# Optimization experiments

Measured on AMD Instinct MI355X. Metric: run time of the kernel, lower is better.

## Reference

```python
import jax, jax.numpy as jnp
import numpy as np

IN_F, OUT_F = 128, 128
R, LEV, N = 2, 2, 8192
JD = (R - 1) * LEV + 1  # 3 filter levels


def setup_inputs() -> dict:
    key = jax.random.key(0)
    ks = jax.random.split(key, 7)
    x = jax.random.normal(ks[0], (N, IN_F), dtype=jnp.float32)
    d_list = jax.random.uniform(ks[1], (JD, N), dtype=jnp.float32)
    U = jax.random.normal(ks[2], (N, N), dtype=jnp.float32)
    Vt = jax.random.normal(ks[3], (N, N), dtype=jnp.float32)
    # learned params
    bound = float(np.sqrt(6.0 / (IN_F + OUT_F)))  # xavier_uniform
    weight = jax.random.uniform(ks[4], (IN_F, OUT_F), dtype=jnp.float32, minval=-bound, maxval=bound)
    filt = jax.random.uniform(ks[5], (JD, N), dtype=jnp.float32, minval=0.9, maxval=1.1)
    bias = jnp.zeros((OUT_F,), dtype=jnp.float32)
    return {"x": x, "d_list": d_list, "U": U, "Vt": Vt, "weight": weight, "filt": filt, "bias": bias}


def reference(x, d_list, U, Vt, weight, filt, bias):
    # Original loop: sum_j U @ ((d_j * f_j * d_j)[:, None] * (Vt @ (x @ W)))
    # By linearity this equals U @ ((sum_j d_j^2 * f_j)[:, None] * (Vt @ (x @ W)))
    # -- same math, with Vt@xw computed once and U applied once.
    xw = x @ weight                                  # [N, out]
    Vxw = Vt @ xw                                    # [N, out]
    scale = jnp.sum(d_list * filt * d_list, axis=0)  # [N]
    out = U @ (scale[:, None] * Vxw)                 # [N, out]
    return out + bias
```

## Files before the change

### kernel.cpp

```cpp
#include <hip/hip_runtime.h>

typedef short s8v __attribute__((ext_vector_type(8)));
typedef float f32x4 __attribute__((ext_vector_type(4)));

#define BM 64
#define KC 64
#define PAD 72

#define LDS_BARRIER() asm volatile("s_waitcnt lgkmcnt(0)\n\ts_barrier" ::: "memory")

__device__ __forceinline__ unsigned short f2bf(float x) {
    unsigned int u = __float_as_uint(x);
    u += 0x7fffu + ((u >> 16) & 1u);
    return (unsigned short)(u >> 16);
}

__global__ __launch_bounds__(256, 2) void gemm_kernel(
    const float* __restrict__ A, int lda,
    const unsigned short* __restrict__ Bt, int ldb,
    float* __restrict__ C, int klen)
{
    __shared__ __align__(16) unsigned short As[2][BM * PAD];
    __shared__ __align__(16) unsigned short Bs[2][128 * PAD];

    const int t    = threadIdx.x;
    const int w    = t >> 6;
    const int lane = t & 63;
    const int quad = lane >> 4;
    const int l16  = lane & 15;
    const int w32  = w * 32;
    const int kq   = quad * 8;

    const int mbase = blockIdx.x * BM;
    const int k0    = blockIdx.y * klen;
    C += (size_t)blockIdx.y * gridDim.x * BM * 128;

    const int ar = t >> 2;
    const int ak = (t & 3) * 16;
    const int br = t >> 1;
    const int bk = (t & 1) * 32;
    const float*          Ap = A  + (size_t)(mbase + ar) * lda + k0 + ak;
    const unsigned short* Bp = Bt + (size_t)br * ldb + k0 + bk;

    const int nchunks = klen / KC;

    float4 a_r[2][4];
    s8v    b_r[2][4];

    {
        #pragma unroll
        for (int i = 0; i < 4; ++i) a_r[0][i] = *(const float4*)(Ap + i * 4);
        #pragma unroll
        for (int i = 0; i < 4; ++i) b_r[0][i] = *(const s8v*)(Bp + i * 8);
        s8v v0, v1;
        v0[0] = (short)f2bf(a_r[0][0].x); v0[1] = (short)f2bf(a_r[0][0].y);
        v0[2] = (short)f2bf(a_r[0][0].z); v0[3] = (short)f2bf(a_r[0][0].w);
        v0[4] = (short)f2bf(a_r[0][1].x); v0[5] = (short)f2bf(a_r[0][1].y);
        v0[6] = (short)f2bf(a_r[0][1].z); v0[7] = (short)f2bf(a_r[0][1].w);
        v1[0] = (short)f2bf(a_r[0][2].x); v1[1] = (short)f2bf(a_r[0][2].y);
        v1[2] = (short)f2bf(a_r[0][2].z); v1[3] = (short)f2bf(a_r[0][2].w);
        v1[4] = (short)f2bf(a_r[0][3].x); v1[5] = (short)f2bf(a_r[0][3].y);
        v1[6] = (short)f2bf(a_r[0][3].z); v1[7] = (short)f2bf(a_r[0][3].w);
        *(s8v*)&As[0][ar * PAD + ak]     = v0;
        *(s8v*)&As[0][ar * PAD + ak + 8] = v1;
        #pragma unroll
        for (int i = 0; i < 4; ++i) *(s8v*)&Bs[0][br * PAD + bk + 8 * i] = b_r[0][i];
        if (nchunks > 1) {
            #pragma unroll
            for (int i = 0; i < 4; ++i) a_r[1][i] = *(const float4*)(Ap + KC + i * 4);
            #pragma unroll
            for (int i = 0; i < 4; ++i) b_r[1][i] = *(const s8v*)(Bp + KC + i * 8);
        }
    }
    LDS_BARRIER();

    f32x4 acc[4][2];
    #pragma unroll
    for (int rt = 0; rt < 4; ++rt)
        #pragma unroll
        for (int ct = 0; ct < 2; ++ct)
            acc[rt][ct] = (f32x4){0.f, 0.f, 0.f, 0.f};

#define GITER(p)                                                               \
    {                                                                          \
        if (c + 2 < nchunks) {                     \
            const size_t o = (size_t)(c + 2) * KC;                             \
            _Pragma("unroll")                                                  \
            for (int i = 0; i < 4; ++i) a_r[p][i] = *(const float4*)(Ap + o + i * 4); \
            _Pragma("unroll")                                                  \
            for (int i = 0; i < 4; ++i) b_r[p][i] = *(const s8v*)(Bp + o + i * 8);    \
        }                                                                      \
        {                                                \
            const unsigned short* as = As[p];                                  \
            const unsigned short* bs = Bs[p];                                  \
            _Pragma("unroll")                                                  \
            for (int kk = 0; kk < 2; ++kk) {                                   \
                const int ko = kk * 32 + kq;                                   \
                s8v af[4], bf[2];                                              \
                _Pragma("unroll")                                              \
                for (int rt = 0; rt < 4; ++rt)                                 \
                    af[rt] = *(const s8v*)&as[(rt * 16 + l16) * PAD + ko];     \
                _Pragma("unroll")                                              \
                for (int ct = 0; ct < 2; ++ct)                                 \
                    bf[ct] = *(const s8v*)&bs[(w32 + ct * 16 + l16) * PAD + ko]; \
                _Pragma("unroll")                                              \
                for (int rt = 0; rt < 4; ++rt)                                 \
                    _Pragma("unroll")                                          \
                    for (int ct = 0; ct < 2; ++ct)                             \
                        acc[rt][ct] = __builtin_amdgcn_mfma_f32_16x16x32_bf16( \
                            af[rt], bf[ct], acc[rt][ct], 0, 0, 0);             \
            }                                                                  \
        }                                                                      \
        if (c + 1 < nchunks) {   \
            const int q = (p) ^ 1;                                             \
            s8v v0, v1;                                                        \
            v0[0] = (short)f2bf(a_r[q][0].x); v0[1] = (short)f2bf(a_r[q][0].y);\
            v0[2] = (short)f2bf(a_r[q][0].z); v0[3] = (short)f2bf(a_r[q][0].w);\
            v0[4] = (short)f2bf(a_r[q][1].x); v0[5] = (short)f2bf(a_r[q][1].y);\
            v0[6] = (short)f2bf(a_r[q][1].z); v0[7] = (short)f2bf(a_r[q][1].w);\
            v1[0] = (short)f2bf(a_r[q][2].x); v1[1] = (short)f2bf(a_r[q][2].y);\
            v1[2] = (short)f2bf(a_r[q][2].z); v1[3] = (short)f2bf(a_r[q][2].w);\
            v1[4] = (short)f2bf(a_r[q][3].x); v1[5] = (short)f2bf(a_r[q][3].y);\
            v1[6] = (short)f2bf(a_r[q][3].z); v1[7] = (short)f2bf(a_r[q][3].w);\
            *(s8v*)&As[q][ar * PAD + ak]     = v0;                             \
            *(s8v*)&As[q][ar * PAD + ak + 8] = v1;                             \
            _Pragma("unroll")                                                  \
            for (int i = 0; i < 4; ++i)                                        \
                *(s8v*)&Bs[q][br * PAD + bk + 8 * i] = b_r[q][i];              \
        }                                                                      \
        LDS_BARRIER();                                                         \
    }

    int c = 0;
    while (true) {
        GITER(0)
        if (++c == nchunks) break;
        GITER(1)
        if (++c == nchunks) break;
    }
#undef GITER

    #pragma unroll
    for (int rt = 0; rt < 4; ++rt) {
        const int row = mbase + rt * 16 + quad * 4;
        #pragma unroll
        for (int ct = 0; ct < 2; ++ct) {
            const int col = w32 + ct * 16 + l16;
            #pragma unroll
            for (int i = 0; i < 4; ++i)
                C[(size_t)(row + i) * 128 + col] = acc[rt][ct][i];
        }
    }
}

__global__ __launch_bounds__(256) void tkern(
    const float* __restrict__ a, int nslabs,
    const float* __restrict__ dl, const float* __restrict__ ft,
    unsigned short* __restrict__ out, int nrows, int mode)
{
    __shared__ __align__(16) unsigned short L[128 * PAD];
    const int t    = threadIdx.x;
    const int kb   = blockIdx.x * 64;
    const int kloc = t >> 2;
    const int fseg = (t & 3) * 32;
    const int k    = kb + kloc;
    const size_t slab = (size_t)nrows * 128;

    float s = 1.0f;
    if (mode) {
        float s0 = 0.f;
        #pragma unroll
        for (int j = 0; j < 3; ++j) {
            float d = dl[(size_t)j * nrows + k];
            s0 += d * d * ft[(size_t)j * nrows + k];
        }
        s = s0;
    }
    const float* ap = a + (size_t)k * 128 + fseg;
    #pragma unroll
    for (int i = 0; i < 8; ++i) {
        float4 v = *(const float4*)(ap + i * 4);
        for (int sl = 1; sl < nslabs; ++sl) {
            float4 u = *(const float4*)(ap + sl * slab + i * 4);
            v.x += u.x; v.y += u.y; v.z += u.z; v.w += u.w;
        }
        const int fb = fseg + i * 4;
        L[(fb + 0) * PAD + kloc] = f2bf(v.x * s);
        L[(fb + 1) * PAD + kloc] = f2bf(v.y * s);
        L[(fb + 2) * PAD + kloc] = f2bf(v.z * s);
        L[(fb + 3) * PAD + kloc] = f2bf(v.w * s);
    }
    __syncthreads();
    const int f    = t >> 1;
    const int half = (t & 1) * 32;
    unsigned short* op = out + (size_t)f * nrows + kb + half;
    #pragma unroll
    for (int i = 0; i < 4; ++i) {
        *(s8v*)(op + i * 8) = *(const s8v*)&L[f * PAD + half + i * 8];
    }
}

__global__ __launch_bounds__(256) void addbias_kernel(
    const float* __restrict__ p, const float* __restrict__ bias,
    float* __restrict__ out)
{
    const size_t e = ((size_t)blockIdx.x * 256 + threadIdx.x) * 4;
    const size_t slab = (size_t)8192 * 128;
    float4 r = *(const float4*)(bias + (e & 127));
    #pragma unroll
    for (int s = 0; s < 4; ++s) {
        float4 x = *(const float4*)(p + s * slab + e);
        r.x += x.x; r.y += x.y; r.z += x.z; r.w += x.w;
    }
    *(float4*)(out + e) = r;
}

extern "C" void kernel_launch(void* const* d_in, const int* in_sizes, int n_in,
                              void* d_out, int out_size, void* d_ws, size_t ws_size,
                              hipStream_t stream)
{
    const float* x  = (const float*)d_in[0];
    const float* dl = (const float*)d_in[1];
    const float* U  = (const float*)d_in[2];
    const float* Vt = (const float*)d_in[3];
    const float* W  = (const float*)d_in[4];
    const float* ft = (const float*)d_in[5];
    const float* bs = (const float*)d_in[6];
    float* out = (float*)d_out;

    const int N = 8192, F = 128;
    const int SPLITK = 4;
    char* ws = (char*)d_ws;
    unsigned short* Wt  = (unsigned short*)(ws);
    unsigned short* xwt = (unsigned short*)(ws + (64 << 10));
    unsigned short* yt  = (unsigned short*)(ws + (64 << 10) + (2 << 20));
    float* bufA = (float*)(ws + (64 << 10) + (4 << 20));
    float* bufB = (float*)(ws + (64 << 10) + (20 << 20));

    tkern<<<dim3(F / 64), 256, 0, stream>>>(W, 1, nullptr, nullptr, Wt, F, 0);
    gemm_kernel<<<dim3(N / BM, 1), 256, 0, stream>>>(x, F, Wt, F, bufA, F);
    tkern<<<dim3(N / 64), 256, 0, stream>>>(bufA, 1, nullptr, nullptr, xwt, N, 0);
    gemm_kernel<<<dim3(N / BM, SPLITK), 256, 0, stream>>>(Vt, N, xwt, N, bufB, N / SPLITK);
    tkern<<<dim3(N / 64), 256, 0, stream>>>(bufB, SPLITK, dl, ft, yt, N, 1);
    gemm_kernel<<<dim3(N / BM, SPLITK), 256, 0, stream>>>(U, N, yt, N, bufA, N / SPLITK);
    addbias_kernel<<<dim3((N * F) / (256 * 4)), 256, 0, stream>>>(bufA, bs, out);
}
```

Measured before the change: 611.9 us.

## Load GEMM fragments directly from global memory and fuse xW transpose epilogue

The GEMM kernel stops staging A and B tiles through LDS with barriers. Each wave now loads its MFMA fragments straight from global memory into registers, double-buffered, and converts A to bf16 in registers; the wave layout changes to a 2x2 split of the 64x128 tile. The x@W GEMM gets its own kernel that writes bf16 transposed output directly, which removes one transpose launch and one fp32 round trip. The trade-off is that B fragments are now read redundantly by each wave, and the global accesses are less coalesced (16 rows with 32-byte segments), all for a GEMM whose cost is dominated by streaming A at 256MB.

```diff
diff --git a/kernel.cpp b/kernel.cpp
--- a/kernel.cpp
+++ b/kernel.cpp
@@ -2,12 +2,10 @@
 
 typedef short s8v __attribute__((ext_vector_type(8)));
 typedef float f32x4 __attribute__((ext_vector_type(4)));
-
-#define BM 64
+typedef unsigned short u16x4 __attribute__((ext_vector_type(4)));
+
 #define KC 64
 #define PAD 72
-
-#define LDS_BARRIER() asm volatile("s_waitcnt lgkmcnt(0)\n\ts_barrier" ::: "memory")
 
 __device__ __forceinline__ unsigned short f2bf(float x) {
     unsigned int u = __float_as_uint(x);
@@ -15,140 +13,143 @@
     return (unsigned short)(u >> 16);
 }
 
-__global__ __launch_bounds__(256, 2) void gemm_kernel(
+__device__ __forceinline__ s8v cvt_frag(const float4 lo, const float4 hi) {
+    s8v r;
+    r[0] = (short)f2bf(lo.x); r[1] = (short)f2bf(lo.y);
+    r[2] = (short)f2bf(lo.z); r[3] = (short)f2bf(lo.w);
+    r[4] = (short)f2bf(hi.x); r[5] = (short)f2bf(hi.y);
+    r[6] = (short)f2bf(hi.z); r[7] = (short)f2bf(hi.w);
+    return r;
+}
+
+__device__ __forceinline__ void gemm_core(
     const float* __restrict__ A, int lda,
     const unsigned short* __restrict__ Bt, int ldb,
-    float* __restrict__ C, int klen)
-{
-    __shared__ __align__(16) unsigned short As[2][BM * PAD];
-    __shared__ __align__(16) unsigned short Bs[2][128 * PAD];
-
+    int mbase, int k0, int klen, f32x4 acc[2][4])
+{
     const int t    = threadIdx.x;
     const int w    = t >> 6;
     const int lane = t & 63;
     const int quad = lane >> 4;
     const int l16  = lane & 15;
-    const int w32  = w * 32;
-    const int kq   = quad * 8;
-
-    const int mbase = blockIdx.x * BM;
-    const int k0    = blockIdx.y * klen;
-    C += (size_t)blockIdx.y * gridDim.x * BM * 128;
-
-    const int ar = t >> 2;
-    const int ak = (t & 3) * 16;
-    const int br = t >> 1;
-    const int bk = (t & 1) * 32;
-    const float*          Ap = A  + (size_t)(mbase + ar) * lda + k0 + ak;
-    const unsigned short* Bp = Bt + (size_t)br * ldb + k0 + bk;
-
+    const int mh   = w >> 1;
+    const int nh   = w & 1;
+
+    const float* rA0 = A + (size_t)(mbase + mh * 32 + l16) * lda + k0 + quad * 8;
+    const float* rA1 = rA0 + (size_t)16 * lda;
+    const unsigned short* rB = Bt + (size_t)(nh * 64 + l16) * ldb + k0 + quad * 8;
+    const size_t bstep = (size_t)16 * ldb;
+
+    float4 a[2][2][2][2];
+    s8v    b[2][2][4];
     const int nchunks = klen / KC;
 
-    float4 a_r[2][4];
-    s8v    b_r[2][4];
-
-    {
-        #pragma unroll
-        for (int i = 0; i < 4; ++i) a_r[0][i] = *(const float4*)(Ap + i * 4);
-        #pragma unroll
-        for (int i = 0; i < 4; ++i) b_r[0][i] = *(const s8v*)(Bp + i * 8);
-        s8v v0, v1;
-        v0[0] = (short)f2bf(a_r[0][0].x); v0[1] = (short)f2bf(a_r[0][0].y);
-        v0[2] = (short)f2bf(a_r[0][0].z); v0[3] = (short)f2bf(a_r[0][0].w);
-        v0[4] = (short)f2bf(a_r[0][1].x); v0[5] = (short)f2bf(a_r[0][1].y);
-        v0[6] = (short)f2bf(a_r[0][1].z); v0[7] = (short)f2bf(a_r[0][1].w);
-        v1[0] = (short)f2bf(a_r[0][2].x); v1[1] = (short)f2bf(a_r[0][2].y);
-        v1[2] = (short)f2bf(a_r[0][2].z); v1[3] = (short)f2bf(a_r[0][2].w);
-        v1[4] = (short)f2bf(a_r[0][3].x); v1[5] = (short)f2bf(a_r[0][3].y);
-        v1[6] = (short)f2bf(a_r[0][3].z); v1[7] = (short)f2bf(a_r[0][3].w);
-        *(s8v*)&As[0][ar * PAD + ak]     = v0;
-        *(s8v*)&As[0][ar * PAD + ak + 8] = v1;
-        #pragma unroll
-        for (int i = 0; i < 4; ++i) *(s8v*)&Bs[0][br * PAD + bk + 8 * i] = b_r[0][i];
-        if (nchunks > 1) {
-            #pragma unroll
-            for (int i = 0; i < 4; ++i) a_r[1][i] = *(const float4*)(Ap + KC + i * 4);
-            #pragma unroll
-            for (int i = 0; i < 4; ++i) b_r[1][i] = *(const s8v*)(Bp + KC + i * 8);
-        }
-    }
-    LDS_BARRIER();
-
-    f32x4 acc[4][2];
-    #pragma unroll
-    for (int rt = 0; rt < 4; ++rt)
-        #pragma unroll
-        for (int ct = 0; ct < 2; ++ct)
-            acc[rt][ct] = (f32x4){0.f, 0.f, 0.f, 0.f};
-
-#define GITER(p)                                                               \
+#define LOADC(s, c) do { const size_t o = (size_t)(c) * KC;                    \
+        _Pragma("unroll")                                                      \
+        for (int kk = 0; kk < 2; ++kk) {                                       \
+            a[s][0][kk][0] = *(const float4*)(rA0 + o + kk * 32);              \
+            a[s][0][kk][1] = *(const float4*)(rA0 + o + kk * 32 + 4);          \
+            a[s][1][kk][0] = *(const float4*)(rA1 + o + kk * 32);              \
+            a[s][1][kk][1] = *(const float4*)(rA1 + o + kk * 32 + 4);          \
+        }                                                                      \
+        _Pragma("unroll")                                                      \
+        for (int kk = 0; kk < 2; ++kk)                                         \
+            _Pragma("unroll")                                                  \
+            for (int ct = 0; ct < 4; ++ct)                                     \
+                b[s][kk][ct] = *(const s8v*)(rB + ct * bstep + o + kk * 32);   \
+    } while (0)
+
+#define ITER(p)                                                                \
     {                                                                          \
-        if (c + 2 < nchunks) {                     \
-            const size_t o = (size_t)(c + 2) * KC;                             \
+        _Pragma("unroll")                                                      \
+        for (int kk = 0; kk < 2; ++kk) {                                       \
+            s8v af0 = cvt_frag(a[p][0][kk][0], a[p][0][kk][1]);                \
+            s8v af1 = cvt_frag(a[p][1][kk][0], a[p][1][kk][1]);                \
             _Pragma("unroll")                                                  \
-            for (int i = 0; i < 4; ++i) a_r[p][i] = *(const float4*)(Ap + o + i * 4); \
-            _Pragma("unroll")                                                  \
-            for (int i = 0; i < 4; ++i) b_r[p][i] = *(const s8v*)(Bp + o + i * 8);    \
-        }                                                                      \
-        {                                                \
-            const unsigned short* as = As[p];                                  \
-            const unsigned short* bs = Bs[p];                                  \
-            _Pragma("unroll")                                                  \
-            for (int kk = 0; kk < 2; ++kk) {                                   \
-                const int ko = kk * 32 + kq;                                   \
-                s8v af[4], bf[2];                                              \
-                _Pragma("unroll")                                              \
-                for (int rt = 0; rt < 4; ++rt)                                 \
-                    af[rt] = *(const s8v*)&as[(rt * 16 + l16) * PAD + ko];     \
-                _Pragma("unroll")                                              \
-                for (int ct = 0; ct < 2; ++ct)                                 \
-                    bf[ct] = *(const s8v*)&bs[(w32 + ct * 16 + l16) * PAD + ko]; \
-                _Pragma("unroll")                                              \
-                for (int rt = 0; rt < 4; ++rt)                                 \
-                    _Pragma("unroll")                                          \
-                    for (int ct = 0; ct < 2; ++ct)                             \
-                        acc[rt][ct] = __builtin_amdgcn_mfma_f32_16x16x32_bf16( \
-                            af[rt], bf[ct], acc[rt][ct], 0, 0, 0);             \
+            for (int ct = 0; ct < 4; ++ct) {                                   \
+                acc[0][ct] = __builtin_amdgcn_mfma_f32_16x16x32_bf16(          \
+                    af0, b[p][kk][ct], acc[0][ct], 0, 0, 0);                   \
+                acc[1][ct] = __builtin_amdgcn_mfma_f32_16x16x32_bf16(          \
+                    af1, b[p][kk][ct], acc[1][ct], 0, 0, 0);                   \
             }                                                                  \
         }                                                                      \
-        if (c + 1 < nchunks) {   \
-            const int q = (p) ^ 1;                                             \
-            s8v v0, v1;                                                        \
-            v0[0] = (short)f2bf(a_r[q][0].x); v0[1] = (short)f2bf(a_r[q][0].y);\
-            v0[2] = (short)f2bf(a_r[q][0].z); v0[3] = (short)f2bf(a_r[q][0].w);\
-            v0[4] = (short)f2bf(a_r[q][1].x); v0[5] = (short)f2bf(a_r[q][1].y);\
-            v0[6] = (short)f2bf(a_r[q][1].z); v0[7] = (short)f2bf(a_r[q][1].w);\
-            v1[0] = (short)f2bf(a_r[q][2].x); v1[1] = (short)f2bf(a_r[q][2].y);\
-            v1[2] = (short)f2bf(a_r[q][2].z); v1[3] = (short)f2bf(a_r[q][2].w);\
-            v1[4] = (short)f2bf(a_r[q][3].x); v1[5] = (short)f2bf(a_r[q][3].y);\
-            v1[6] = (short)f2bf(a_r[q][3].z); v1[7] = (short)f2bf(a_r[q][3].w);\
-            *(s8v*)&As[q][ar * PAD + ak]     = v0;                             \
-            *(s8v*)&As[q][ar * PAD + ak + 8] = v1;                             \
-            _Pragma("unroll")                                                  \
-            for (int i = 0; i < 4; ++i)                                        \
-                *(s8v*)&Bs[q][br * PAD + bk + 8 * i] = b_r[q][i];              \
-        }                                                                      \
-        LDS_BARRIER();                                                         \
-    }
-
+        if (c + 2 < nchunks) LOADC(p, c + 2);                                  \
+    }
+
+    LOADC(0, 0);
+    if (nchunks > 1) LOADC(1, 1);
     int c = 0;
     while (true) {
-        GITER(0)
+        ITER(0)
         if (++c == nchunks) break;
-        GITER(1)
+        ITER(1)
         if (++c == nchunks) break;
     }
-#undef GITER
-
-    #pragma unroll
-    for (int rt = 0; rt < 4; ++rt) {
-        const int row = mbase + rt * 16 + quad * 4;
-        #pragma unroll
-        for (int ct = 0; ct < 2; ++ct) {
-            const int col = w32 + ct * 16 + l16;
+#undef ITER
+#undef LOADC
+}
+
+__global__ __launch_bounds__(256, 2) void gemm_kernel(
+    const float* __restrict__ A, int lda,
+    const unsigned short* __restrict__ Bt, int ldb,
+    float* __restrict__ C, int klen)
+{
+    f32x4 acc[2][4];
+    #pragma unroll
+    for (int rt = 0; rt < 2; ++rt)
+        #pragma unroll
+        for (int ct = 0; ct < 4; ++ct)
+            acc[rt][ct] = (f32x4){0.f, 0.f, 0.f, 0.f};
+
+    const int mbase = blockIdx.x * 64;
+    gemm_core(A, lda, Bt, ldb, mbase, blockIdx.y * klen, klen, acc);
+
+    C += (size_t)blockIdx.y * 8192 * 128;
+    const int t = threadIdx.x;
+    const int lane = t & 63, w = t >> 6;
+    const int quad = lane >> 4, l16 = lane & 15;
+    const int mh = w >> 1, nh = w & 1;
+    #pragma unroll
+    for (int rt = 0; rt < 2; ++rt) {
+        const int row0 = mbase + mh * 32 + rt * 16 + quad * 4;
+        #pragma unroll
+        for (int ct = 0; ct < 4; ++ct) {
+            const int col = nh * 64 + ct * 16 + l16;
             #pragma unroll
             for (int i = 0; i < 4; ++i)
-                C[(size_t)(row + i) * 128 + col] = acc[rt][ct][i];
+                C[(size_t)(row0 + i) * 128 + col] = acc[rt][ct][i];
+        }
+    }
+}
+
+__global__ __launch_bounds__(256, 2) void gemm_xw_kernel(
+    const float* __restrict__ x, const unsigned short* __restrict__ Wt,
+    unsigned short* __restrict__ out)
+{
+    f32x4 acc[2][4];
+    #pragma unroll
+    for (int rt = 0; rt < 2; ++rt)
+        #pragma unroll
+        for (int ct = 0; ct < 4; ++ct)
+            acc[rt][ct] = (f32x4){0.f, 0.f, 0.f, 0.f};
+
+    const int mbase = blockIdx.x * 64;
+    gemm_core(x, 128, Wt, 128, mbase, 0, 128, acc);
+
+    const int t = threadIdx.x;
+    const int lane = t & 63, w = t >> 6;
+    const int quad = lane >> 4, l16 = lane & 15;
+    const int mh = w >> 1, nh = w & 1;
+    #pragma unroll
+    for (int rt = 0; rt < 2; ++rt) {
+        const int r0 = mbase + mh * 32 + rt * 16 + quad * 4;
+        #pragma unroll
+        for (int ct = 0; ct < 4; ++ct) {
+            const int f = nh * 64 + ct * 16 + l16;
+            u16x4 v;
+            v[0] = f2bf(acc[rt][ct][0]); v[1] = f2bf(acc[rt][ct][1]);
+            v[2] = f2bf(acc[rt][ct][2]); v[3] = f2bf(acc[rt][ct][3]);
+            *(u16x4*)&out[(size_t)f * 8192 + r0] = v;
         }
     }
 }
@@ -228,7 +229,7 @@
     const float* bs = (const float*)d_in[6];
     float* out = (float*)d_out;
 
-    const int N = 8192, F = 128;
+    const int N = 8192;
     const int SPLITK = 4;
     char* ws = (char*)d_ws;
     unsigned short* Wt  = (unsigned short*)(ws);
@@ -237,11 +238,10 @@
     float* bufA = (float*)(ws + (64 << 10) + (4 << 20));
     float* bufB = (float*)(ws + (64 << 10) + (20 << 20));
 
-    tkern<<<dim3(F / 64), 256, 0, stream>>>(W, 1, nullptr, nullptr, Wt, F, 0);
-    gemm_kernel<<<dim3(N / BM, 1), 256, 0, stream>>>(x, F, Wt, F, bufA, F);
-    tkern<<<dim3(N / 64), 256, 0, stream>>>(bufA, 1, nullptr, nullptr, xwt, N, 0);
-    gemm_kernel<<<dim3(N / BM, SPLITK), 256, 0, stream>>>(Vt, N, xwt, N, bufB, N / SPLITK);
+    tkern<<<dim3(2), 256, 0, stream>>>(W, 1, nullptr, nullptr, Wt, 128, 0);
+    gemm_xw_kernel<<<dim3(N / 64), 256, 0, stream>>>(x, Wt, xwt);
+    gemm_kernel<<<dim3(N / 64, SPLITK), 256, 0, stream>>>(Vt, N, xwt, N, bufB, N / SPLITK);
     tkern<<<dim3(N / 64), 256, 0, stream>>>(bufB, SPLITK, dl, ft, yt, N, 1);
-    gemm_kernel<<<dim3(N / BM, SPLITK), 256, 0, stream>>>(U, N, yt, N, bufA, N / SPLITK);
-    addbias_kernel<<<dim3((N * F) / (256 * 4)), 256, 0, stream>>>(bufA, bs, out);
-}
+    gemm_kernel<<<dim3(N / 64, SPLITK), 256, 0, stream>>>(U, N, yt, N, bufA, N / SPLITK);
+    addbias_kernel<<<dim3((N * 128) / (256 * 4)), 256, 0, stream>>>(bufA, bs, out);
+}
```

Result: slower. 671.8 us (+9.8%).
